# Performance work log

Measured on AMD Instinct MI355X. Metric: run time of the kernel, lower is better.

## Reference

```python
import jax, jax.numpy as jnp
import numpy as np
import math

N_NODES = 50000
N_EDGES = 1600000
DIM = 64
HEADS = 8
EDGE_DIM = 32


def setup_inputs() -> dict:
    key = jax.random.key(0)
    ks = jax.random.split(key, 12)
    s = 1.0 / math.sqrt(DIM)
    se = 1.0 / math.sqrt(EDGE_DIM)
    return {
        'x': jax.random.normal(ks[0], (N_NODES, DIM), jnp.float32),
        'edge_index': jax.random.randint(ks[1], (2, N_EDGES), 0, N_NODES),
        'edge_attr': jax.random.normal(ks[2], (N_EDGES, EDGE_DIM), jnp.float32),
        'WQ': jax.random.normal(ks[3], (DIM, DIM), jnp.float32) * s,
        'bQ': jnp.zeros((DIM,), jnp.float32),
        'WK': jax.random.normal(ks[4], (DIM, DIM), jnp.float32) * s,
        'bK': jnp.zeros((DIM,), jnp.float32),
        'WV': jax.random.normal(ks[5], (DIM, DIM), jnp.float32) * s,
        'bV': jnp.zeros((DIM,), jnp.float32),
        'WO': jax.random.normal(ks[6], (DIM, DIM), jnp.float32) * s,
        'bO': jnp.zeros((DIM,), jnp.float32),
        'We1': jax.random.normal(ks[7], (EDGE_DIM, EDGE_DIM), jnp.float32) * se,
        'be1': jnp.zeros((EDGE_DIM,), jnp.float32),
        'We2': jax.random.normal(ks[8], (EDGE_DIM, HEADS), jnp.float32) * se,
        'be2': jnp.zeros((HEADS,), jnp.float32),
    }


def graph_softmax(src, index, num_segments):
    # src: [E, H], index: [E] -> per-destination-node stable softmax
    smax = jax.ops.segment_max(src, index, num_segments=num_segments)  # [N, H]
    smax = jnp.where(jnp.isfinite(smax), smax, 0.0)  # nodes with no edges
    e = jnp.exp(src - smax[index])
    ssum = jax.ops.segment_sum(e, index, num_segments=num_segments) + 1e-12
    return e / ssum[index]


def reference(x, edge_index, edge_attr, WQ, bQ, WK, bK, WV, bV, WO, bO, We1, be1, We2, be2):
    num_nodes = x.shape[0]
    d_k = DIM // HEADS
    i, j = edge_index[0], edge_index[1]
    # per-node projections [N, H, d_k], then gather per-edge
    Q = (x @ WQ + bQ).reshape(num_nodes, HEADS, d_k)
    K = (x @ WK + bK).reshape(num_nodes, HEADS, d_k)
    V = (x @ WV + bV).reshape(num_nodes, HEADS, d_k)
    query = Q[j]  # [E, H, d_k]
    key = K[i]
    value = V[i]
    # edge bias MLP: [edge_dim -> edge_dim -> num_heads] with SiLU between
    h = jax.nn.silu(edge_attr @ We1 + be1)
    bias = h @ We2 + be2  # [E, H]
    scores = jnp.sum(query * key, axis=-1) / math.sqrt(d_k) + bias  # [E, H]
    alpha = graph_softmax(scores, j, num_nodes)  # [E, H]
    weighted = (alpha[..., None] * value).reshape(-1, DIM)  # [E, dim]
    attn_out = jax.ops.segment_sum(weighted, j, num_segments=num_nodes)  # [N, dim]
    return attn_out @ WO + bO
```

## Files before the change

### kernel.cpp

```cpp
#include <hip/hip_runtime.h>
#include <math.h>

#define N_NODES 50000
#define N_EDGES 1600000
#define DIM 64
#define HEADS 8
#define EDGE_DIM 32

#define NB 256
#define NPB 196
#define ACAP 8192
#define PART_T 256
#define EPT 4
#define PART_E (PART_T * EPT)

#define QKV_BLKS 12500

typedef __fp16 h2 __attribute__((ext_vector_type(2)));

__device__ __forceinline__ unsigned int f2bf(float f) {
    union { float f; unsigned int u; } c; c.f = f;
    unsigned int u = c.u;
    return (u + 0x7FFFu + ((u >> 16) & 1u)) >> 16;
}
__device__ __forceinline__ float bf_lo(unsigned int u) { return __uint_as_float(u << 16); }
__device__ __forceinline__ float bf_hi(unsigned int u) { return __uint_as_float(u & 0xFFFF0000u); }

__global__ __launch_bounds__(1024) void pack_weights(
    const float* __restrict__ We1, const float* __restrict__ We2,
    h2* __restrict__ w1p, h2* __restrict__ w2p, int* __restrict__ gcur)
{
    const int t = threadIdx.x;
    if (t < 512) {
        const int c = t >> 4, kk = t & 15;
        w1p[t] = __builtin_amdgcn_cvt_pkrtz(We1[(2 * kk) * EDGE_DIM + c],
                                            We1[(2 * kk + 1) * EDGE_DIM + c]);
    } else if (t < 512 + 128) {
        const int u = t - 512;
        const int h = u >> 4, cc = u & 15;
        w2p[u] = __builtin_amdgcn_cvt_pkrtz(We2[(2 * cc) * HEADS + h],
                                            We2[(2 * cc + 1) * HEADS + h]);
    } else if (t >= 768 && t < 768 + NB) {
        gcur[t - 768] = 0;
    }
}

__global__ __launch_bounds__(256) void mlp_partition(
    const int* __restrict__ ei,
    const float* __restrict__ edge_attr,
    const h2* __restrict__ w1p, const float* __restrict__ be1,
    const h2* __restrict__ w2p, const float* __restrict__ be2,
    int* __restrict__ gcur,
    uint2* __restrict__ A_rec, uint4* __restrict__ bias_by_e)
{
    __shared__ int cnt[NB];
    __shared__ int base[NB];
    __shared__ int lbase[NB];
    __shared__ int total_s;
    __shared__ uint2 srec[PART_E];
    __shared__ unsigned char sbkt[PART_E];
    const int tid = threadIdx.x;
    cnt[tid] = 0;
    __syncthreads();
    const int e0 = blockIdx.x * PART_E;
    #pragma unroll
    for (int k = 0; k < EPT; ++k) {
        const int e = e0 + k * PART_T + tid;
        if (e < N_EDGES) atomicAdd(&cnt[ei[N_EDGES + e] / NPB], 1);
    }
    __syncthreads();
    lbase[tid] = cnt[tid];
    __syncthreads();
    for (int o = 1; o < NB; o <<= 1) {
        int t = (tid >= o) ? lbase[tid - o] : 0;
        __syncthreads();
        lbase[tid] += t;
        __syncthreads();
    }
    {
        const int inc = lbase[tid];
        const int c = cnt[tid];
        base[tid] = (c > 0) ? atomicAdd(&gcur[tid], c) : 0;
        lbase[tid] = inc - c;
        if (tid == NB - 1) total_s = inc;
        cnt[tid] = 0;
    }
    __syncthreads();
    for (int k = 0; k < EPT; ++k) {
        const int e = e0 + k * PART_T + tid;
        if (e >= N_EDGES) break;
        const int i = ei[e];
        const int j = ei[N_EDGES + e];
        const int b = j / NPB;
        const int jl = j - b * NPB;
        float a[EDGE_DIM];
        const float4* ar = (const float4*)(edge_attr + (size_t)e * EDGE_DIM);
        #pragma unroll
        for (int q = 0; q < EDGE_DIM / 4; ++q) {
            float4 v = ar[q];
            a[q * 4 + 0] = v.x; a[q * 4 + 1] = v.y;
            a[q * 4 + 2] = v.z; a[q * 4 + 3] = v.w;
        }
        h2 a2[EDGE_DIM / 2];
        #pragma unroll
        for (int kk = 0; kk < EDGE_DIM / 2; ++kk)
            a2[kk] = __builtin_amdgcn_cvt_pkrtz(a[2 * kk], a[2 * kk + 1]);
        float sil[EDGE_DIM];
        #pragma unroll 8
        for (int c = 0; c < EDGE_DIM; ++c) {
            float s = be1[c];
            #pragma unroll
            for (int kk = 0; kk < EDGE_DIM / 2; ++kk)
                s = __builtin_amdgcn_fdot2(a2[kk], w1p[c * 16 + kk], s, false);
            sil[c] = __fdividef(s, 1.0f + __expf(-s));
        }
        h2 s2[EDGE_DIM / 2];
        #pragma unroll
        for (int cc = 0; cc < EDGE_DIM / 2; ++cc)
            s2[cc] = __builtin_amdgcn_cvt_pkrtz(sil[2 * cc], sil[2 * cc + 1]);
        float b0f = be2[0], b1f = be2[1], b2f = be2[2], b3f = be2[3];
        float b4f = be2[4], b5f = be2[5], b6f = be2[6], b7f = be2[7];
        #pragma unroll
        for (int cc = 0; cc < EDGE_DIM / 2; ++cc) {
            b0f = __builtin_amdgcn_fdot2(s2[cc], w2p[0 * 16 + cc], b0f, false);
            b1f = __builtin_amdgcn_fdot2(s2[cc], w2p[1 * 16 + cc], b1f, false);
            b2f = __builtin_amdgcn_fdot2(s2[cc], w2p[2 * 16 + cc], b2f, false);
            b3f = __builtin_amdgcn_fdot2(s2[cc], w2p[3 * 16 + cc], b3f, false);
            b4f = __builtin_amdgcn_fdot2(s2[cc], w2p[4 * 16 + cc], b4f, false);
            b5f = __builtin_amdgcn_fdot2(s2[cc], w2p[5 * 16 + cc], b5f, false);
            b6f = __builtin_amdgcn_fdot2(s2[cc], w2p[6 * 16 + cc], b6f, false);
            b7f = __builtin_amdgcn_fdot2(s2[cc], w2p[7 * 16 + cc], b7f, false);
        }
        uint4 br;
        br.x = f2bf(b0f) | (f2bf(b1f) << 16);
        br.y = f2bf(b2f) | (f2bf(b3f) << 16);
        br.z = f2bf(b4f) | (f2bf(b5f) << 16);
        br.w = f2bf(b6f) | (f2bf(b7f) << 16);
        bias_by_e[e] = br;
        const int s = lbase[b] + atomicAdd(&cnt[b], 1);
        srec[s] = make_uint2((unsigned)e, ((unsigned)jl << 24) | (unsigned)i);
        sbkt[s] = (unsigned char)b;
    }
    __syncthreads();
    const int total = total_s;
    for (int s = tid; s < total; s += PART_T) {
        const int b = sbkt[s];
        const int gp = base[b] + (s - lbase[b]);
        if (gp < ACAP) A_rec[(size_t)b * ACAP + gp] = srec[s];
    }
}

__global__ __launch_bounds__(256) void perm_qkv(
    const int* __restrict__ gcur, const uint2* __restrict__ A_rec,
    int* __restrict__ offs, uint2* __restrict__ es_sorted,
    const float* __restrict__ x,
    const float* __restrict__ WQ, const float* __restrict__ bQ,
    const float* __restrict__ WK, const float* __restrict__ bK,
    const float* __restrict__ WV, const float* __restrict__ bV,
    float* __restrict__ Q, unsigned int* __restrict__ KV)
{
    __shared__ __align__(16) char smem[3 * DIM * DIM * sizeof(float)];
    const int tid = threadIdx.x;
    if (blockIdx.x < NB) {
        int* sc   = (int*)smem;
        int* ldeg = sc + NB;
        int* loff = ldeg + NPB;
        int* gb   = loff + NPB + 1;
        const int b = blockIdx.x;
        sc[tid] = min(gcur[tid], ACAP);
        __syncthreads();
        for (int o = 1; o < NB; o <<= 1) {
            int t = (tid >= o) ? sc[tid - o] : 0;
            __syncthreads();
            sc[tid] += t;
            __syncthreads();
        }
        if (tid == 0) gb[0] = (b == 0) ? 0 : sc[b - 1];
        if (tid < NPB) ldeg[tid] = 0;
        __syncthreads();
        const int gbase = gb[0];
        const int nb = min(gcur[b], ACAP);
        for (int r = tid; r < nb; r += 256)
            atomicAdd(&ldeg[A_rec[(size_t)b * ACAP + r].y >> 24], 1);
        __syncthreads();
        sc[tid] = (tid < NPB) ? ldeg[tid] : 0;
        __syncthreads();
        for (int o = 1; o < 256; o <<= 1) {
            int t = (tid >= o) ? sc[tid - o] : 0;
            __syncthreads();
            sc[tid] += t;
            __syncthreads();
        }
        if (tid == 0) loff[0] = 0;
        if (tid < NPB) { loff[tid + 1] = sc[tid]; ldeg[tid] = 0; }
        __syncthreads();
        const int jbase = b * NPB;
        if (tid < NPB && jbase + tid < N_NODES) offs[jbase + tid] = gbase + loff[tid];
        if (b == NB - 1 && tid == 0) offs[N_NODES] = gbase + nb;
        for (int r = tid; r < nb; r += 256) {
            const uint2 rec = A_rec[(size_t)b * ACAP + r];
            const int jl = (int)(rec.y >> 24);
            const int slot = loff[jl] + atomicAdd(&ldeg[jl], 1);
            es_sorted[(size_t)gbase + slot] = make_uint2(rec.x, rec.y & 0xFFFFFFu);
        }
    } else {
        float* sWQ = (float*)smem;
        float* sWK = sWQ + DIM * DIM;
        float* sWV = sWK + DIM * DIM;
        for (int t = tid; t < DIM * DIM; t += 256) {
            sWQ[t] = WQ[t]; sWK[t] = WK[t]; sWV[t] = WV[t];
        }
        __syncthreads();
        const int lane = tid & 63;
        const int wave = tid >> 6;
        const int n = (blockIdx.x - NB) * 4 + wave;
        if (n >= N_NODES) return;
        float xl = x[(size_t)n * DIM + lane];
        float aq = bQ[lane], ak = bK[lane], av = bV[lane];
        #pragma unroll
        for (int k = 0; k < DIM; ++k) {
            float xv = __shfl(xl, k, 64);
            aq += xv * sWQ[k * DIM + lane];
            ak += xv * sWK[k * DIM + lane];
            av += xv * sWV[k * DIM + lane];
        }
        Q[(size_t)n * DIM + lane] = aq;
        KV[(size_t)n * DIM + lane] = f2bf(ak) | (f2bf(av) << 16);
    }
}

__global__ __launch_bounds__(256) void node_attn_out(
    const int* __restrict__ off,
    const uint2* __restrict__ es_sorted,
    const unsigned short* __restrict__ bias_u16,
    const float* __restrict__ Q, const unsigned int* __restrict__ KV,
    const float* __restrict__ WO, const float* __restrict__ bO,
    float* __restrict__ out)
{
    __shared__ float sWO[DIM * DIM];
    for (int t = threadIdx.x; t < DIM * DIM; t += 256) sWO[t] = WO[t];
    __syncthreads();
    const int lane = threadIdx.x & 63;
    const int wave = threadIdx.x >> 6;
    const int j = blockIdx.x * 4 + wave;
    if (j >= N_NODES) return;
    const int beg = off[j], end = off[j + 1];
    const int h = lane >> 3;
    const float qv = Q[(size_t)j * DIM + lane];
    const float inv_sqrt_dk = 0.35355339059327373f;
    float num = 0.0f;
    float den = 1e-12f;
    int t = beg;
    for (; t + 7 < end; t += 8) {
        uint2 r[8];
        unsigned int u[8];
        float bb[8], d[8];
        #pragma unroll
        for (int q = 0; q < 8; ++q) r[q] = es_sorted[t + q];
        #pragma unroll
        for (int q = 0; q < 8; ++q) u[q] = KV[(size_t)r[q].y * DIM + lane];
        #pragma unroll
        for (int q = 0; q < 8; ++q)
            bb[q] = bf_lo((unsigned int)bias_u16[(size_t)r[q].x * HEADS + h]);
        #pragma unroll
        for (int q = 0; q < 8; ++q) d[q] = qv * bf_lo(u[q]);
        #pragma unroll
        for (int q = 0; q < 8; ++q) d[q] += __shfl_xor(d[q], 1, 64);
        #pragma unroll
        for (int q = 0; q < 8; ++q) d[q] += __shfl_xor(d[q], 2, 64);
        #pragma unroll
        for (int q = 0; q < 8; ++q) d[q] += __shfl_xor(d[q], 4, 64);
        #pragma unroll
        for (int q = 0; q < 8; ++q) {
            const float ev = __expf(d[q] * inv_sqrt_dk + bb[q]);
            num += ev * bf_hi(u[q]);
            den += ev;
        }
    }
    for (; t + 3 < end; t += 4) {
        uint2 r[4];
        unsigned int u[4];
        float bb[4], d[4];
        #pragma unroll
        for (int q = 0; q < 4; ++q) r[q] = es_sorted[t + q];
        #pragma unroll
        for (int q = 0; q < 4; ++q) u[q] = KV[(size_t)r[q].y * DIM + lane];
        #pragma unroll
        for (int q = 0; q < 4; ++q)
            bb[q] = bf_lo((unsigned int)bias_u16[(size_t)r[q].x * HEADS + h]);
        #pragma unroll
        for (int q = 0; q < 4; ++q) d[q] = qv * bf_lo(u[q]);
        #pragma unroll
        for (int q = 0; q < 4; ++q) d[q] += __shfl_xor(d[q], 1, 64);
        #pragma unroll
        for (int q = 0; q < 4; ++q) d[q] += __shfl_xor(d[q], 2, 64);
        #pragma unroll
        for (int q = 0; q < 4; ++q) d[q] += __shfl_xor(d[q], 4, 64);
        #pragma unroll
        for (int q = 0; q < 4; ++q) {
            const float ev = __expf(d[q] * inv_sqrt_dk + bb[q]);
            num += ev * bf_hi(u[q]);
            den += ev;
        }
    }
    for (; t < end; ++t) {
        const uint2 r0 = es_sorted[t];
        const unsigned int u0 = KV[(size_t)r0.y * DIM + lane];
        const float b0 = bf_lo((unsigned int)bias_u16[(size_t)r0.x * HEADS + h]);
        float d0 = qv * bf_lo(u0);
        d0 += __shfl_xor(d0, 1, 64);
        d0 += __shfl_xor(d0, 2, 64);
        d0 += __shfl_xor(d0, 4, 64);
        const float e0 = __expf(d0 * inv_sqrt_dk + b0);
        num += e0 * bf_hi(u0);
        den += e0;
    }
    const float av = num / den;
    float acc = bO[lane];
    #pragma unroll
    for (int k = 0; k < DIM; ++k) {
        acc += __shfl(av, k, 64) * sWO[k * DIM + lane];
    }
    out[(size_t)j * DIM + lane] = acc;
}

extern "C" void kernel_launch(void* const* d_in, const int* in_sizes, int n_in,
                              void* d_out, int out_size, void* d_ws, size_t ws_size,
                              hipStream_t stream) {
    const float* x    = (const float*)d_in[0];
    const int*   ei   = (const int*)d_in[1];
    const float* ea   = (const float*)d_in[2];
    const float* WQ   = (const float*)d_in[3];
    const float* bQ   = (const float*)d_in[4];
    const float* WK   = (const float*)d_in[5];
    const float* bK   = (const float*)d_in[6];
    const float* WV   = (const float*)d_in[7];
    const float* bV   = (const float*)d_in[8];
    const float* WO   = (const float*)d_in[9];
    const float* bO   = (const float*)d_in[10];
    const float* We1  = (const float*)d_in[11];
    const float* be1  = (const float*)d_in[12];
    const float* We2  = (const float*)d_in[13];
    const float* be2  = (const float*)d_in[14];
    float* out = (float*)d_out;

    char* ws = (char*)d_ws;
    size_t off_b = 0;
    auto alloc = [&](size_t bytes) {
        void* p = ws + off_b;
        off_b += (bytes + 255) & ~(size_t)255;
        return p;
    };
    float*        Q         = (float*)alloc((size_t)N_NODES * DIM * sizeof(float));
    unsigned int* KV        = (unsigned int*)alloc((size_t)N_NODES * DIM * sizeof(unsigned int));
    uint2*        A_rec     = (uint2*)alloc((size_t)NB * ACAP * sizeof(uint2));
    uint4*        bias_by_e = (uint4*)alloc((size_t)N_EDGES * sizeof(uint4));
    uint2*        es_sorted = (uint2*)alloc((size_t)N_EDGES * sizeof(uint2));
    int*          offs      = (int*)alloc((size_t)(N_NODES + 1) * sizeof(int));
    int*          gcur      = (int*)alloc((size_t)NB * sizeof(int));
    h2*           w1p       = (h2*)alloc(512 * sizeof(h2));
    h2*           w2p       = (h2*)alloc(128 * sizeof(h2));

    pack_weights<<<1, 1024, 0, stream>>>(We1, We2, w1p, w2p, gcur);
    mlp_partition<<<(N_EDGES + PART_E - 1) / PART_E, PART_T, 0, stream>>>(
        ei, ea, w1p, be1, w2p, be2, gcur, A_rec, bias_by_e);
    perm_qkv<<<NB + QKV_BLKS, 256, 0, stream>>>(gcur, A_rec, offs, es_sorted,
                                                x, WQ, bQ, WK, bK, WV, bV, Q, KV);
    node_attn_out<<<(N_NODES + 3) / 4, 256, 0, stream>>>(offs, es_sorted,
                                                         (const unsigned short*)bias_by_e,
                                                         Q, KV, WO, bO, out);
}
```

Measured before the change: 325.4 us.

## Pack Q/K as fp16 pairs and process two edges per wave in attention

Q and K are stored as packed fp16 pairs and V as packed bf16 pairs in a new per-node layout (K half, V half). The attention kernel splits each wave into two 32-lane halves that each handle a different edge, using fdot2 for the Q·K product and one fewer shuffle stage. Partial sums are combined across halves at the end. This halves Q storage and per-edge instruction count, at the cost of lower Q/K precision (fp16) and two separate 128-byte gathers per edge.

```diff
diff --git a/kernel.cpp b/kernel.cpp
--- a/kernel.cpp
+++ b/kernel.cpp
@@ -25,6 +25,8 @@
 }
 __device__ __forceinline__ float bf_lo(unsigned int u) { return __uint_as_float(u << 16); }
 __device__ __forceinline__ float bf_hi(unsigned int u) { return __uint_as_float(u & 0xFFFF0000u); }
+__device__ __forceinline__ unsigned int h2u(h2 v) { union { h2 h; unsigned int u; } c; c.h = v; return c.u; }
+__device__ __forceinline__ h2 u2h(unsigned int x) { union { h2 h; unsigned int u; } c; c.u = x; return c.h; }
 
 __global__ __launch_bounds__(1024) void pack_weights(
     const float* __restrict__ We1, const float* __restrict__ We2,
@@ -157,7 +159,7 @@
     const float* __restrict__ WQ, const float* __restrict__ bQ,
     const float* __restrict__ WK, const float* __restrict__ bK,
     const float* __restrict__ WV, const float* __restrict__ bV,
-    float* __restrict__ Q, unsigned int* __restrict__ KV)
+    unsigned int* __restrict__ Q2, unsigned int* __restrict__ KV2)
 {
     __shared__ __align__(16) char smem[3 * DIM * DIM * sizeof(float)];
     const int tid = threadIdx.x;
@@ -224,8 +226,19 @@
             ak += xv * sWK[k * DIM + lane];
             av += xv * sWV[k * DIM + lane];
         }
-        Q[(size_t)n * DIM + lane] = aq;
-        KV[(size_t)n * DIM + lane] = f2bf(ak) | (f2bf(av) << 16);
+        const int s = lane & 31;
+        const float aq_e = __shfl(aq, 2 * s, 64);
+        const float aq_o = __shfl(aq, 2 * s + 1, 64);
+        const float ak_e = __shfl(ak, 2 * s, 64);
+        const float ak_o = __shfl(ak, 2 * s + 1, 64);
+        const float av_e = __shfl(av, 2 * s, 64);
+        const float av_o = __shfl(av, 2 * s + 1, 64);
+        if (lane < 32) {
+            Q2[(size_t)n * 32 + s]  = h2u(__builtin_amdgcn_cvt_pkrtz(aq_e, aq_o));
+            KV2[(size_t)n * 64 + s] = h2u(__builtin_amdgcn_cvt_pkrtz(ak_e, ak_o));
+        } else {
+            KV2[(size_t)n * 64 + 32 + s] = f2bf(av_e) | (f2bf(av_o) << 16);
+        }
     }
 }
 
@@ -233,7 +246,7 @@
     const int* __restrict__ off,
     const uint2* __restrict__ es_sorted,
     const unsigned short* __restrict__ bias_u16,
-    const float* __restrict__ Q, const unsigned int* __restrict__ KV,
+    const unsigned int* __restrict__ Q2, const unsigned int* __restrict__ KV2,
     const float* __restrict__ WO, const float* __restrict__ bO,
     float* __restrict__ out)
 {
@@ -245,81 +258,79 @@
     const int j = blockIdx.x * 4 + wave;
     if (j >= N_NODES) return;
     const int beg = off[j], end = off[j + 1];
-    const int h = lane >> 3;
-    const float qv = Q[(size_t)j * DIM + lane];
+    const int s = lane & 31;
+    const int half = lane >> 5;
+    const int h = s >> 2;
     const float inv_sqrt_dk = 0.35355339059327373f;
-    float num = 0.0f;
+    const h2 q2 = u2h(Q2[(size_t)j * 32 + s]);
+    float num2x = 0.0f, num2y = 0.0f;
     float den = 1e-12f;
     int t = beg;
     for (; t + 7 < end; t += 8) {
-        uint2 r[8];
-        unsigned int u[8];
-        float bb[8], d[8];
-        #pragma unroll
-        for (int q = 0; q < 8; ++q) r[q] = es_sorted[t + q];
-        #pragma unroll
-        for (int q = 0; q < 8; ++q) u[q] = KV[(size_t)r[q].y * DIM + lane];
-        #pragma unroll
-        for (int q = 0; q < 8; ++q)
-            bb[q] = bf_lo((unsigned int)bias_u16[(size_t)r[q].x * HEADS + h]);
-        #pragma unroll
-        for (int q = 0; q < 8; ++q) d[q] = qv * bf_lo(u[q]);
-        #pragma unroll
-        for (int q = 0; q < 8; ++q) d[q] += __shfl_xor(d[q], 1, 64);
-        #pragma unroll
-        for (int q = 0; q < 8; ++q) d[q] += __shfl_xor(d[q], 2, 64);
-        #pragma unroll
-        for (int q = 0; q < 8; ++q) d[q] += __shfl_xor(d[q], 4, 64);
-        #pragma unroll
-        for (int q = 0; q < 8; ++q) {
-            const float ev = __expf(d[q] * inv_sqrt_dk + bb[q]);
-            num += ev * bf_hi(u[q]);
-            den += ev;
-        }
-    }
-    for (; t + 3 < end; t += 4) {
         uint2 r[4];
-        unsigned int u[4];
+        unsigned int k2v[4], v2v[4];
         float bb[4], d[4];
         #pragma unroll
-        for (int q = 0; q < 4; ++q) r[q] = es_sorted[t + q];
-        #pragma unroll
-        for (int q = 0; q < 4; ++q) u[q] = KV[(size_t)r[q].y * DIM + lane];
+        for (int q = 0; q < 4; ++q) r[q] = es_sorted[t + 2 * q + half];
+        #pragma unroll
+        for (int q = 0; q < 4; ++q) k2v[q] = KV2[(size_t)r[q].y * 64 + s];
+        #pragma unroll
+        for (int q = 0; q < 4; ++q) v2v[q] = KV2[(size_t)r[q].y * 64 + 32 + s];
         #pragma unroll
         for (int q = 0; q < 4; ++q)
             bb[q] = bf_lo((unsigned int)bias_u16[(size_t)r[q].x * HEADS + h]);
         #pragma unroll
-        for (int q = 0; q < 4; ++q) d[q] = qv * bf_lo(u[q]);
+        for (int q = 0; q < 4; ++q)
+            d[q] = __builtin_amdgcn_fdot2(q2, u2h(k2v[q]), 0.0f, false);
         #pragma unroll
         for (int q = 0; q < 4; ++q) d[q] += __shfl_xor(d[q], 1, 64);
         #pragma unroll
         for (int q = 0; q < 4; ++q) d[q] += __shfl_xor(d[q], 2, 64);
-        #pragma unroll
-        for (int q = 0; q < 4; ++q) d[q] += __shfl_xor(d[q], 4, 64);
         #pragma unroll
         for (int q = 0; q < 4; ++q) {
             const float ev = __expf(d[q] * inv_sqrt_dk + bb[q]);
-            num += ev * bf_hi(u[q]);
+            num2x += ev * bf_lo(v2v[q]);
+            num2y += ev * bf_hi(v2v[q]);
             den += ev;
         }
     }
-    for (; t < end; ++t) {
+    for (; t + 1 < end; t += 2) {
+        const uint2 r0 = es_sorted[t + half];
+        const unsigned int k2v = KV2[(size_t)r0.y * 64 + s];
+        const unsigned int v2v = KV2[(size_t)r0.y * 64 + 32 + s];
+        const float bb = bf_lo((unsigned int)bias_u16[(size_t)r0.x * HEADS + h]);
+        float d = __builtin_amdgcn_fdot2(q2, u2h(k2v), 0.0f, false);
+        d += __shfl_xor(d, 1, 64);
+        d += __shfl_xor(d, 2, 64);
+        const float ev = __expf(d * inv_sqrt_dk + bb);
+        num2x += ev * bf_lo(v2v);
+        num2y += ev * bf_hi(v2v);
+        den += ev;
+    }
+    if (t < end) {
         const uint2 r0 = es_sorted[t];
-        const unsigned int u0 = KV[(size_t)r0.y * DIM + lane];
-        const float b0 = bf_lo((unsigned int)bias_u16[(size_t)r0.x * HEADS + h]);
-        float d0 = qv * bf_lo(u0);
-        d0 += __shfl_xor(d0, 1, 64);
-        d0 += __shfl_xor(d0, 2, 64);
-        d0 += __shfl_xor(d0, 4, 64);
-        const float e0 = __expf(d0 * inv_sqrt_dk + b0);
-        num += e0 * bf_hi(u0);
-        den += e0;
-    }
-    const float av = num / den;
+        const unsigned int k2v = KV2[(size_t)r0.y * 64 + s];
+        const unsigned int v2v = KV2[(size_t)r0.y * 64 + 32 + s];
+        const float bb = bf_lo((unsigned int)bias_u16[(size_t)r0.x * HEADS + h]);
+        float d = __builtin_amdgcn_fdot2(q2, u2h(k2v), 0.0f, false);
+        d += __shfl_xor(d, 1, 64);
+        d += __shfl_xor(d, 2, 64);
+        float ev = __expf(d * inv_sqrt_dk + bb);
+        if (half != 0) ev = 0.0f;
+        num2x += ev * bf_lo(v2v);
+        num2y += ev * bf_hi(v2v);
+        den += ev;
+    }
+    num2x += __shfl_xor(num2x, 32, 64);
+    num2y += __shfl_xor(num2y, 32, 64);
+    den   += __shfl_xor(den, 32, 64);
+    const float av2x = num2x / den;
+    const float av2y = num2y / den;
     float acc = bO[lane];
     #pragma unroll
-    for (int k = 0; k < DIM; ++k) {
-        acc += __shfl(av, k, 64) * sWO[k * DIM + lane];
+    for (int sp = 0; sp < 32; ++sp) {
+        acc += __shfl(av2x, sp, 64) * sWO[(2 * sp) * DIM + lane];
+        acc += __shfl(av2y, sp, 64) * sWO[(2 * sp + 1) * DIM + lane];
     }
     out[(size_t)j * DIM + lane] = acc;
 }
@@ -351,8 +362,8 @@
         off_b += (bytes + 255) & ~(size_t)255;
         return p;
     };
-    float*        Q         = (float*)alloc((size_t)N_NODES * DIM * sizeof(float));
-    unsigned int* KV        = (unsigned int*)alloc((size_t)N_NODES * DIM * sizeof(unsigned int));
+    unsigned int* Q2        = (unsigned int*)alloc((size_t)N_NODES * 32 * sizeof(unsigned int));
+    unsigned int* KV2       = (unsigned int*)alloc((size_t)N_NODES * 64 * sizeof(unsigned int));
     uint2*        A_rec     = (uint2*)alloc((size_t)NB * ACAP * sizeof(uint2));
     uint4*        bias_by_e = (uint4*)alloc((size_t)N_EDGES * sizeof(uint4));
     uint2*        es_sorted = (uint2*)alloc((size_t)N_EDGES * sizeof(uint2));
@@ -365,8 +376,8 @@
     mlp_partition<<<(N_EDGES + PART_E - 1) / PART_E, PART_T, 0, stream>>>(
         ei, ea, w1p, be1, w2p, be2, gcur, A_rec, bias_by_e);
     perm_qkv<<<NB + QKV_BLKS, 256, 0, stream>>>(gcur, A_rec, offs, es_sorted,
-                                                x, WQ, bQ, WK, bK, WV, bV, Q, KV);
+                                                x, WQ, bQ, WK, bK, WV, bV, Q2, KV2);
     node_attn_out<<<(N_NODES + 3) / 4, 256, 0, stream>>>(offs, es_sorted,
                                                          (const unsigned short*)bias_by_e,
-                                                         Q, KV, WO, bO, out);
-}
+                                                         Q2, KV2, WO, bO, out);
+}
```

After: 303.7 us. -6.7%, faster.
